# Performance work log

Hardware: AMD Instinct MI355X
Metric: run time of the kernel (lower is better)

## Reference

```python
import jax, jax.numpy as jnp
import numpy as np

B, S, DIM, H = 2, 2048, 1024, 16
DH = DIM // H


def setup_inputs() -> dict:
    key = jax.random.key(0)
    ks = jax.random.split(key, 12)
    sd = 0.02
    inp = {
        "query": jax.random.normal(ks[0], (B, S, DIM), jnp.float32),
        "key": jax.random.normal(ks[1], (B, S, DIM), jnp.float32),
        "value": jax.random.normal(ks[2], (B, S, DIM), jnp.float32),
        "pad_mask": jax.random.randint(ks[3], (B, 1, 1, S), 0, 2, jnp.int32),
        "training_status": 1,
        "Wq": jax.random.normal(ks[4], (DIM, DIM), jnp.float32) * sd,
        "bq": jnp.zeros((DIM,), jnp.float32),
        "Wk": jax.random.normal(ks[5], (DIM, DIM), jnp.float32) * sd,
        "bk": jnp.zeros((DIM,), jnp.float32),
        "Wv": jax.random.normal(ks[6], (DIM, DIM), jnp.float32) * sd,
        "bv": jnp.zeros((DIM,), jnp.float32),
        "Wf": jax.random.normal(ks[7], (DIM, DIM), jnp.float32) * sd,
        "bf": jnp.zeros((DIM,), jnp.float32),
    }
    return inp


def reference(query, key, value, pad_mask, training_status, Wq, bq, Wk, bk, Wv, bv, Wf, bf):
    b, s, _ = query.shape
    # projections, split heads -> [B, H, S, Dh]
    def split_heads(x):
        return x.reshape(b, -1, H, DH).transpose(0, 2, 1, 3)

    q = split_heads(query @ Wq + bq)
    k = split_heads(key @ Wk + bk)
    v = split_heads(value @ Wv + bv)

    # NOTE: original divides by sqrt(Dh) twice (explicit + self.scale) => /Dh
    scores = jnp.einsum("bhqd,bhkd->bhqk", q, k) / jnp.asarray(DH, q.dtype)
    if training_status:
        scores = jnp.where(pad_mask == 0, jnp.asarray(-1e9, scores.dtype), scores)
    attn = jax.nn.softmax(scores, axis=-1)
    out = jnp.einsum("bhqk,bhkd->bhqd", attn, v)  # [B,H,S,Dh]
    out = out.transpose(0, 2, 1, 3).reshape(b, s, DIM)
    return out @ Wf + bf
```

## Files before the change

### kernel.cpp

```cpp
#include <hip/hip_runtime.h>

#define Bn   2
#define Sn   2048
#define DIMn 1024
#define Hn   16
#define DHn  64

typedef unsigned short u16;
typedef unsigned int   u32;

typedef __attribute__((ext_vector_type(8))) __bf16 bf16x8;
typedef __attribute__((ext_vector_type(8))) float  f32x8v;
typedef __attribute__((ext_vector_type(4))) float  f32x4;

__device__ __forceinline__ u16 f2bf(float f) {
    union { float f; u32 u; } v; v.f = f;
    u32 r = v.u + 0x7fffu + ((v.u >> 16) & 1u);
    return (u16)(r >> 16);
}
__device__ __forceinline__ bf16x8 ldfrag(const u16* p) {
    union { uint4 u; bf16x8 v; } x;
    x.u = *(const uint4*)p;
    return x.v;
}
__device__ __forceinline__ uint4 pack8(const u16 h[8]) {
    uint4 r;
    r.x = (u32)h[0] | ((u32)h[1] << 16);
    r.y = (u32)h[2] | ((u32)h[3] << 16);
    r.z = (u32)h[4] | ((u32)h[5] << 16);
    r.w = (u32)h[6] | ((u32)h[7] << 16);
    return r;
}
__device__ __forceinline__ void gl_lds16(const void* g, void* l) {
    __builtin_amdgcn_global_load_lds(
        (const __attribute__((address_space(1))) void*)g,
        (__attribute__((address_space(3))) void*)l, 16, 0, 0);
}
__device__ __forceinline__ void barrier_nodrain() {
    asm volatile("" ::: "memory");
    __builtin_amdgcn_s_barrier();
    asm volatile("" ::: "memory");
}

__global__ __launch_bounds__(256) void prep_weights(
    const float* __restrict__ Wq, const float* __restrict__ Wk,
    const float* __restrict__ Wv, const float* __restrict__ Wf,
    u16* __restrict__ Wt)
{
    __shared__ __align__(16) float tile[64][68];
    const float* W = (blockIdx.z == 0) ? Wq : (blockIdx.z == 1) ? Wk
                   : (blockIdx.z == 2) ? Wv : Wf;
    u16* out = Wt + (size_t)blockIdx.z * DIMn * DIMn;
    const int t = threadIdx.x;
    const int n0 = blockIdx.x * 64, k0 = blockIdx.y * 64;
    const int rr = t >> 4, cc = (t & 15) * 4;
#pragma unroll
    for (int i = 0; i < 4; i++)
        *(float4*)&tile[rr + 16 * i][cc] =
            *(const float4*)(W + (size_t)(k0 + rr + 16 * i) * DIMn + n0 + cc);
    __syncthreads();
#pragma unroll
    for (int e = 0; e < 2; e++) {
        const int ci = 2 * t + e;
        const int n = ci >> 3, kc = ci & 7;
        u16 h[8];
#pragma unroll
        for (int j = 0; j < 8; j++) h[j] = f2bf(tile[kc * 8 + j][n]);
        *(uint4*)(out + (size_t)(n0 + n) * DIMn + k0 + kc * 8) = pack8(h);
    }
}

__global__ __launch_bounds__(256) void gemm_qkv(
    const float* __restrict__ Aq, const float* __restrict__ Ak,
    const float* __restrict__ Av, const u16* __restrict__ Wt,
    const float* __restrict__ bqp, const float* __restrict__ bkp,
    const float* __restrict__ bvp, u16* __restrict__ Qw,
    u16* __restrict__ Kw, u16* __restrict__ VwT)
{
    __shared__ union {
        struct { __align__(16) float Afp[2][64 * 64];
                 __align__(16) u16   Bbf[2][32 * 128]; } s;
        __align__(16) u16 Ep[32][144];
    } L;

    const int f = blockIdx.x;
    const int xcd = f & 7;
    const int q = f >> 3;
    const int z = q >> 5;
    const int rem = q & 31;
    const int yi = rem >> 3, x = rem & 7;
    const int y = xcd * 4 + yi;
    const int m0 = y * 128, n0 = x * 128;

    const float* A    = (z == 0) ? Aq  : (z == 1) ? Ak  : Av;
    const float* bias = (z == 0) ? bqp : (z == 1) ? bkp : bvp;
    const u16* Bt = Wt + (size_t)z * DIMn * DIMn;

    const int t = threadIdx.x;
    const int lane = t & 63, wave = t >> 6;
    const int quad = lane >> 4, l15 = lane & 15;
    const int wm = wave >> 1, wn = wave & 1;

    const float* baseA[4];
#pragma unroll
    for (int s = 0; s < 4; s++) {
        const int c = wave * 16 + s * 4 + quad;
        const int g = c >> 3, qq = (c >> 1) & 3, h = c & 1;
        baseA[s] = A + (size_t)(m0 + g * 16 + l15) * DIMn + qq * 8 + h * 4;
    }
    const u16* baseB[2];
#pragma unroll
    for (int s = 0; s < 2; s++) {
        const int c = wave * 8 + s * 4 + quad;
        const int jg = c >> 2, qq = c & 3;
        baseB[s] = Bt + (size_t)(n0 + jg * 16 + l15) * DIMn + qq * 8;
    }

    auto STAGE = [&](int tt, int buf) {
        const int k0 = tt * 32;
#pragma unroll
        for (int s = 0; s < 4; s++)
            gl_lds16(baseA[s] + k0, &L.s.Afp[buf][(wave * 16 + s * 4) * 64]);
#pragma unroll
        for (int s = 0; s < 2; s++)
            gl_lds16(baseB[s] + k0, &L.s.Bbf[buf][(wave * 8 + s * 4) * 128]);
    };

    f32x4 acc[4][4];
#pragma unroll
    for (int i = 0; i < 4; i++)
#pragma unroll
        for (int j = 0; j < 4; j++) acc[i][j] = (f32x4){0.f, 0.f, 0.f, 0.f};

    const int NT = DIMn / 32;
    STAGE(0, 0);
    STAGE(1, 1);

#pragma unroll 2
    for (int tt = 0; tt < NT; ++tt) {
        const int buf = tt & 1;
        if (tt < NT - 1) asm volatile("s_waitcnt vmcnt(6)" ::: "memory");
        else             asm volatile("s_waitcnt vmcnt(0)" ::: "memory");
        barrier_nodrain();

        bf16x8 a[4], b[4];
#pragma unroll
        for (int i = 0; i < 4; i++) {
            const int g = wm * 4 + i;
            union { struct { f32x4 lo, hi; } p; f32x8v v; } u;
            u.p.lo = *(const f32x4*)&L.s.Afp[buf][(g * 8 + quad * 2 + 0) * 64 + l15 * 4];
            u.p.hi = *(const f32x4*)&L.s.Afp[buf][(g * 8 + quad * 2 + 1) * 64 + l15 * 4];
            a[i] = __builtin_convertvector(u.v, bf16x8);
        }
#pragma unroll
        for (int j = 0; j < 4; j++)
            b[j] = ldfrag(&L.s.Bbf[buf][((wn * 4 + j) * 4 + quad) * 128 + l15 * 8]);
#pragma unroll
        for (int i = 0; i < 4; i++)
#pragma unroll
            for (int j = 0; j < 4; j++)
                acc[i][j] = __builtin_amdgcn_mfma_f32_16x16x32_bf16(a[i], b[j], acc[i][j], 0, 0, 0);

        asm volatile("s_waitcnt lgkmcnt(0)" ::: "memory");
        barrier_nodrain();
        if (tt + 2 < NT) STAGE(tt + 2, buf);
    }

    float bv[4];
#pragma unroll
    for (int j = 0; j < 4; j++) bv[j] = bias[n0 + wn * 64 + j * 16 + l15];

    const int bb = y >> 4;

    if (z < 2) {
        u16* out = (z == 0) ? Qw : Kw;
#pragma unroll
        for (int i = 0; i < 4; i++) {
            __syncthreads();
#pragma unroll
            for (int j = 0; j < 4; j++)
#pragma unroll
                for (int r = 0; r < 4; r++)
                    L.Ep[wm * 16 + quad * 4 + r][wn * 64 + j * 16 + l15] =
                        f2bf(acc[i][j][r] + bv[j]);
            __syncthreads();
#pragma unroll
            for (int e = 0; e < 2; e++) {
                const int ci = t + 256 * e;
                const int row = ci >> 4, c = ci & 15;
                const uint4 v = *(const uint4*)&L.Ep[row][c * 8];
                const int m = m0 + (row >> 4) * 64 + i * 16 + (row & 15);
                const int ss = m & 2047;
                const int n = n0 + c * 8;
                const int hh = n >> 6, dd = n & 63;
                *(uint4*)(out + ((size_t)(bb * Hn + hh) * Sn + ss) * DHn + dd) = v;
            }
        }
    } else {
#pragma unroll
        for (int j = 0; j < 4; j++) {
            __syncthreads();
#pragma unroll
            for (int i = 0; i < 4; i++) {
                u16 h4[4];
#pragma unroll
                for (int r = 0; r < 4; r++) h4[r] = f2bf(acc[i][j][r] + bv[j]);
                uint2 pk;
                pk.x = (u32)h4[0] | ((u32)h4[1] << 16);
                pk.y = (u32)h4[2] | ((u32)h4[3] << 16);
                *(uint2*)&L.Ep[wn * 16 + l15][wm * 64 + i * 16 + quad * 4] = pk;
            }
            __syncthreads();
#pragma unroll
            for (int e = 0; e < 2; e++) {
                const int ci = t + 256 * e;
                const int row = ci >> 4, c = ci & 15;
                const uint4 v = *(const uint4*)&L.Ep[row][c * 8];
                const int n = n0 + (row >> 4) * 64 + j * 16 + (row & 15);
                const int hh = n >> 6, dd = n & 63;
                const int ss = (m0 & 2047) + c * 8;
                *(uint4*)(VwT + ((size_t)(bb * Hn + hh) * DHn + dd) * Sn + ss) = v;
            }
        }
    }
}

__global__ __launch_bounds__(256) void gemm_final(
    const u16* __restrict__ A, const u16* __restrict__ Bt,
    const float* __restrict__ bias, float* __restrict__ out)
{
    __shared__ __align__(16) u16 Abf[3][32 * 128];
    __shared__ __align__(16) u16 Bbf[3][32 * 128];

    const int f = blockIdx.x;
    const int xcd = f & 7, q = f >> 3;
    const int y = xcd * 4 + (q >> 3), x = q & 7;
    const int m0 = y * 128, n0 = x * 128;

    const int t = threadIdx.x;
    const int lane = t & 63, wave = t >> 6;
    const int quad = lane >> 4, l15 = lane & 15;
    const int wm = wave >> 1, wn = wave & 1;

    int arow[2], aq[2];
#pragma unroll
    for (int s = 0; s < 2; s++) {
        const int c = wave * 8 + s * 4 + quad;
        arow[s] = (c >> 2) * 16 + l15;
        aq[s] = c & 3;
    }
    const u16* baseB[2];
#pragma unroll
    for (int s = 0; s < 2; s++) {
        const int c = wave * 8 + s * 4 + quad;
        baseB[s] = Bt + (size_t)(n0 + (c >> 2) * 16 + l15) * DIMn + (c & 3) * 8;
    }

    auto STAGE = [&](int tt, int buf) {
        const int hh = tt >> 1, d64 = (tt & 1) * 32;
#pragma unroll
        for (int s = 0; s < 2; s++) {
            const int m = m0 + arow[s], bb = m >> 11, ss = m & 2047;
            const u16* gp = A + ((size_t)(bb * Hn + hh) * Sn + ss) * DHn + d64 + aq[s] * 8;
            gl_lds16(gp, &Abf[buf][(wave * 8 + s * 4) * 128]);
        }
#pragma unroll
        for (int s = 0; s < 2; s++)
            gl_lds16(baseB[s] + tt * 32, &Bbf[buf][(wave * 8 + s * 4) * 128]);
    };

    f32x4 acc[4][4];
#pragma unroll
    for (int i = 0; i < 4; i++)
#pragma unroll
        for (int j = 0; j < 4; j++) acc[i][j] = (f32x4){0.f, 0.f, 0.f, 0.f};

    const int NT = DIMn / 32;
    STAGE(0, 0);
    STAGE(1, 1);
    STAGE(2, 2);

    int buf = 0;
    for (int tt = 0; tt < NT; ++tt) {
        if (tt < NT - 2)       asm volatile("s_waitcnt vmcnt(8)" ::: "memory");
        else if (tt == NT - 2) asm volatile("s_waitcnt vmcnt(4)" ::: "memory");
        else                   asm volatile("s_waitcnt vmcnt(0)" ::: "memory");
        barrier_nodrain();

        bf16x8 a[4], b[4];
#pragma unroll
        for (int i = 0; i < 4; i++)
            a[i] = ldfrag(&Abf[buf][((wm * 4 + i) * 4 + quad) * 128 + l15 * 8]);
#pragma unroll
        for (int j = 0; j < 4; j++)
            b[j] = ldfrag(&Bbf[buf][((wn * 4 + j) * 4 + quad) * 128 + l15 * 8]);
#pragma unroll
        for (int i = 0; i < 4; i++)
#pragma unroll
            for (int j = 0; j < 4; j++)
                acc[i][j] = __builtin_amdgcn_mfma_f32_16x16x32_bf16(a[i], b[j], acc[i][j], 0, 0, 0);

        asm volatile("s_waitcnt lgkmcnt(0)" ::: "memory");
        barrier_nodrain();
        if (tt + 3 < NT) STAGE(tt + 3, buf);
        buf = (buf == 2) ? 0 : buf + 1;
    }

    float bv[4];
#pragma unroll
    for (int j = 0; j < 4; j++) bv[j] = bias[n0 + wn * 64 + j * 16 + l15];

#pragma unroll
    for (int i = 0; i < 4; i++)
#pragma unroll
        for (int j = 0; j < 4; j++) {
            const int n = n0 + wn * 64 + j * 16 + l15;
#pragma unroll
            for (int r = 0; r < 4; r++) {
                const int m = m0 + wm * 64 + i * 16 + quad * 4 + r;
                out[(size_t)m * DIMn + n] = acc[i][j][r] + bv[j];
            }
        }
}

__global__ __launch_bounds__(256) void attn_mfma(
    const u16* __restrict__ Qw, const u16* __restrict__ Kw,
    const u16* __restrict__ VwT, const int* __restrict__ mask,
    const int* __restrict__ tstat, u16* __restrict__ Aw)
{
    __shared__ __align__(16) u16 Kbf[2][32 * 128];
    __shared__ __align__(16) u16 Vbf[2][32 * 128];
    __shared__ __align__(16) u16 Ps[64 * 64];

    const int f = blockIdx.x;
    const int xcd = f & 7, q = f >> 3;
    const int p = xcd * 4 + (q >> 5);
    const int qt = q & 31;
    const int b = p >> 4, h = p & 15;
    const int q0 = qt * 64;

    const int t = threadIdx.x;
    const int lane = t & 63, wave = t >> 6;
    const int quad = lane >> 4, l15 = lane & 15;
    const bool use_mask = (tstat[0] != 0);
    const size_t slab = (size_t)(b * Hn + h) * Sn * DHn;

    const u16* baseK[2];
    const u16* baseV[2];
#pragma unroll
    for (int s = 0; s < 2; s++) {
        const int c = wave * 8 + s * 4 + quad;
        const int rg = c >> 3, qp = c & 7;
        baseK[s] = Kw  + slab + (size_t)(rg * 16 + l15) * DHn + qp * 8;
        baseV[s] = VwT + slab + (size_t)(rg * 16 + l15) * Sn  + qp * 8;
    }

    {
        const int4* msrc4 = (const int4*)(mask + (size_t)b * Sn);
        int4* mdst4 = (int4*)&Kbf[0][0];
        mdst4[t]       = msrc4[t];
        mdst4[t + 256] = msrc4[t + 256];
    }
    bf16x8 aq[2];
#pragma unroll
    for (int ks = 0; ks < 2; ks++) {
        union { uint4 u; bf16x8 v; } xx;
        xx.u = *(const uint4*)(Qw + slab + (size_t)(q0 + wave * 16 + l15) * DHn + ks * 32 + quad * 8);
        aq[ks] = xx.v;
    }
    __syncthreads();

    u32 mw0 = 0, mw1 = 0, mw2 = 0, mw3 = 0;
    {
        const int* ml = (const int*)&Kbf[0][0];
#pragma unroll
        for (int k = 0; k < 128; k++) {
            const u32 bit = (ml[k * 16 + l15] != 0) ? 1u : 0u;
            if (k < 32)      mw0 |= bit << k;
            else if (k < 64) mw1 |= bit << (k - 32);
            else if (k < 96) mw2 |= bit << (k - 64);
            else             mw3 |= bit << (k - 96);
        }
    }
    __syncthreads();

    auto STAGE = [&](int tt, int buf) {
        const int j0 = tt * 64;
#pragma unroll
        for (int s = 0; s < 2; s++) {
            gl_lds16(baseK[s] + (size_t)j0 * DHn, &Kbf[buf][(wave * 8 + s * 4) * 128]);
            gl_lds16(baseV[s] + j0,               &Vbf[buf][(wave * 8 + s * 4) * 128]);
        }
    };

    float lsum[4] = {0.f, 0.f, 0.f, 0.f};
    f32x4 O[4];
#pragma unroll
    for (int dt = 0; dt < 4; dt++) O[dt] = (f32x4){0.f, 0.f, 0.f, 0.f};

    const int NT = Sn / 64;
    STAGE(0, 0);
    STAGE(1, 1);

#pragma unroll 2
    for (int tt = 0; tt < NT; ++tt) {
        const int buf = tt & 1;
        if (tt < NT - 1) asm volatile("s_waitcnt vmcnt(4)" ::: "memory");
        else             asm volatile("s_waitcnt vmcnt(0)" ::: "memory");
        barrier_nodrain();

        f32x4 s[4];
#pragma unroll
        for (int ct = 0; ct < 4; ct++) s[ct] = (f32x4){0.f, 0.f, 0.f, 0.f};
#pragma unroll
        for (int ct = 0; ct < 4; ct++)
#pragma unroll
            for (int ks = 0; ks < 2; ks++) {
                const bf16x8 bk = ldfrag(&Kbf[buf][(ct * 8 + ks * 4 + quad) * 128 + l15 * 8]);
                s[ct] = __builtin_amdgcn_mfma_f32_16x16x32_bf16(aq[ks], bk, s[ct], 0, 0, 0);
            }

        const int wsel = tt >> 3;
        const u32 cw = (wsel == 0) ? mw0 : (wsel == 1) ? mw1 : (wsel == 2) ? mw2 : mw3;
        const int sh = (tt & 7) * 4;
        u32 mc[4];
#pragma unroll
        for (int ct = 0; ct < 4; ct++)
            mc[ct] = use_mask ? ((cw >> (sh + ct)) & 1u) : 1u;

#pragma unroll
        for (int ct = 0; ct < 4; ct++)
#pragma unroll
            for (int r = 0; r < 4; r++) {
                const float sv = mc[ct] ? s[ct][r] * (1.0f / 64.0f) : -1e9f;
                const float pp = __expf(sv);
                lsum[r] += pp;
                const int prow = wave * 16 + quad * 4 + r;
                Ps[prow * 64 + ((ct * 16 + l15) ^ ((prow & 7) << 3))] = f2bf(pp);
            }
        asm volatile("s_waitcnt lgkmcnt(0)" ::: "memory");

        bf16x8 pa[2];
        const int rrow = wave * 16 + l15;
#pragma unroll
        for (int kc = 0; kc < 2; kc++)
            pa[kc] = ldfrag(&Ps[rrow * 64 + ((kc * 32 + quad * 8) ^ ((l15 & 7) << 3))]);
#pragma unroll
        for (int dt = 0; dt < 4; dt++)
#pragma unroll
            for (int kc = 0; kc < 2; kc++) {
                const bf16x8 bvv = ldfrag(&Vbf[buf][(dt * 8 + kc * 4 + quad) * 128 + l15 * 8]);
                O[dt] = __builtin_amdgcn_mfma_f32_16x16x32_bf16(pa[kc], bvv, O[dt], 0, 0, 0);
            }

        asm volatile("s_waitcnt lgkmcnt(0)" ::: "memory");
        barrier_nodrain();
        if (tt + 2 < NT) STAGE(tt + 2, buf);
    }

#pragma unroll
    for (int r = 0; r < 4; r++) {
#pragma unroll
        for (int off = 1; off < 16; off <<= 1) lsum[r] += __shfl_xor(lsum[r], off);
    }

#pragma unroll
    for (int r = 0; r < 4; r++) {
        const float linv = 1.0f / fmaxf(lsum[r], 1e-30f);
        const int srow = q0 + wave * 16 + quad * 4 + r;
#pragma unroll
        for (int dt = 0; dt < 4; dt++)
            Aw[slab + (size_t)srow * DHn + dt * 16 + l15] = f2bf(O[dt][r] * linv);
    }
}

extern "C" void kernel_launch(void* const* d_in, const int* in_sizes, int n_in,
                              void* d_out, int out_size, void* d_ws, size_t ws_size,
                              hipStream_t stream) {
    const float* query = (const float*)d_in[0];
    const float* key   = (const float*)d_in[1];
    const float* value = (const float*)d_in[2];
    const int*   pmask = (const int*)d_in[3];
    const int*   tstat = (const int*)d_in[4];
    const float* Wq  = (const float*)d_in[5];
    const float* bq  = (const float*)d_in[6];
    const float* Wk  = (const float*)d_in[7];
    const float* bk  = (const float*)d_in[8];
    const float* Wv  = (const float*)d_in[9];
    const float* bv  = (const float*)d_in[10];
    const float* Wf  = (const float*)d_in[11];
    const float* bfb = (const float*)d_in[12];
    float* outp = (float*)d_out;

    const size_t NT = (size_t)Bn * Sn * DIMn;
    u16* Qw  = (u16*)d_ws;
    u16* Kw  = Qw + NT;
    u16* VwT = Kw + NT;
    u16* Wt  = VwT + NT;
    const size_t WSZ = (size_t)DIMn * DIMn;

    prep_weights<<<dim3(16, 16, 4), 256, 0, stream>>>(Wq, Wk, Wv, Wf, Wt);

    gemm_qkv<<<768, 256, 0, stream>>>(query, key, value, Wt, bq, bk, bv, Qw, Kw, VwT);

    attn_mfma<<<1024, 256, 0, stream>>>(Qw, Kw, VwT, pmask, tstat, Qw);

    gemm_final<<<256, 256, 0, stream>>>(Qw, Wt + 3 * WSZ, bfb, outp);
}
```

Baseline: 307.6 us.

## Pre-tile weights, K and V into fragment-contiguous blocks; swizzle A staging; stage attention output

Weights, K and V are now written in a tiled, MFMA-fragment-ordered layout, so each global-to-LDS load in the GEMM and attention kernels reads one contiguous 8KB block per tile instead of strided rows. The fp32 A tile in the QKV GEMM is staged with an XOR swizzle to reduce LDS bank conflicts. The attention epilogue goes through LDS so output rows are written with coalesced 16-byte stores instead of scattered 2-byte stores. The cost is more complex index math in the epilogues, and every producer and consumer must agree on the new layout.

```diff
diff --git a/kernel.cpp b/kernel.cpp
--- a/kernel.cpp
+++ b/kernel.cpp
@@ -50,7 +50,6 @@
     __shared__ __align__(16) float tile[64][68];
     const float* W = (blockIdx.z == 0) ? Wq : (blockIdx.z == 1) ? Wk
                    : (blockIdx.z == 2) ? Wv : Wf;
-    u16* out = Wt + (size_t)blockIdx.z * DIMn * DIMn;
     const int t = threadIdx.x;
     const int n0 = blockIdx.x * 64, k0 = blockIdx.y * 64;
     const int rr = t >> 4, cc = (t & 15) * 4;
@@ -62,11 +61,16 @@
 #pragma unroll
     for (int e = 0; e < 2; e++) {
         const int ci = 2 * t + e;
-        const int n = ci >> 3, kc = ci & 7;
+        const int nn = ci >> 3, kc = ci & 7;
+        const int n = n0 + nn, k = k0 + kc * 8;
         u16 h[8];
 #pragma unroll
-        for (int j = 0; j < 8; j++) h[j] = f2bf(tile[kc * 8 + j][n]);
-        *(uint4*)(out + (size_t)(n0 + n) * DIMn + k0 + kc * 8) = pack8(h);
+        for (int j = 0; j < 8; j++) h[j] = f2bf(tile[kc * 8 + j][nn]);
+        const int X = n >> 7, o = (n >> 4) & 7, l15 = n & 15;
+        const int T = k >> 5, quad = (k >> 3) & 3;
+        const size_t off =
+            ((((size_t)(blockIdx.z * 8 + X) * 32 + T) * 8 + o) * 64 + quad * 16 + l15) * 8;
+        *(uint4*)(Wt + off) = pack8(h);
     }
 }
 
@@ -78,8 +82,8 @@
     u16* __restrict__ Kw, u16* __restrict__ VwT)
 {
     __shared__ union {
-        struct { __align__(16) float Afp[2][64 * 64];
-                 __align__(16) u16   Bbf[2][32 * 128]; } s;
+        struct { __align__(16) float Afp[2][4096];
+                 __align__(16) u16   Bbf[2][4096]; } s;
         __align__(16) u16 Ep[32][144];
     } L;
 
@@ -94,36 +98,29 @@
 
     const float* A    = (z == 0) ? Aq  : (z == 1) ? Ak  : Av;
     const float* bias = (z == 0) ? bqp : (z == 1) ? bkp : bvp;
-    const u16* Bt = Wt + (size_t)z * DIMn * DIMn;
 
     const int t = threadIdx.x;
     const int lane = t & 63, wave = t >> 6;
     const int quad = lane >> 4, l15 = lane & 15;
     const int wm = wave >> 1, wn = wave & 1;
 
+    const int r8 = lane >> 3, c8 = lane & 7;
     const float* baseA[4];
 #pragma unroll
-    for (int s = 0; s < 4; s++) {
-        const int c = wave * 16 + s * 4 + quad;
-        const int g = c >> 3, qq = (c >> 1) & 3, h = c & 1;
-        baseA[s] = A + (size_t)(m0 + g * 16 + l15) * DIMn + qq * 8 + h * 4;
-    }
+    for (int s = 0; s < 4; s++)
+        baseA[s] = A + (size_t)(m0 + (wave * 4 + s) * 8 + r8) * DIMn + ((c8 ^ r8) << 2);
     const u16* baseB[2];
 #pragma unroll
-    for (int s = 0; s < 2; s++) {
-        const int c = wave * 8 + s * 4 + quad;
-        const int jg = c >> 2, qq = c & 3;
-        baseB[s] = Bt + (size_t)(n0 + jg * 16 + l15) * DIMn + qq * 8;
-    }
+    for (int s = 0; s < 2; s++)
+        baseB[s] = Wt + ((size_t)((z * 8 + x) * 32) * 8 + (wave * 2 + s)) * 512 + lane * 8;
 
     auto STAGE = [&](int tt, int buf) {
-        const int k0 = tt * 32;
 #pragma unroll
         for (int s = 0; s < 4; s++)
-            gl_lds16(baseA[s] + k0, &L.s.Afp[buf][(wave * 16 + s * 4) * 64]);
+            gl_lds16(baseA[s] + tt * 32, &L.s.Afp[buf][(wave * 4 + s) * 256]);
 #pragma unroll
         for (int s = 0; s < 2; s++)
-            gl_lds16(baseB[s] + k0, &L.s.Bbf[buf][(wave * 8 + s * 4) * 128]);
+            gl_lds16(baseB[s] + (size_t)tt * 4096, &L.s.Bbf[buf][(wave * 8 + s * 4) * 128]);
     };
 
     f32x4 acc[4][4];
@@ -146,10 +143,11 @@
         bf16x8 a[4], b[4];
 #pragma unroll
         for (int i = 0; i < 4; i++) {
-            const int g = wm * 4 + i;
+            const int lr = wm * 64 + i * 16 + l15;
+            const int rx = lr & 7;
             union { struct { f32x4 lo, hi; } p; f32x8v v; } u;
-            u.p.lo = *(const f32x4*)&L.s.Afp[buf][(g * 8 + quad * 2 + 0) * 64 + l15 * 4];
-            u.p.hi = *(const f32x4*)&L.s.Afp[buf][(g * 8 + quad * 2 + 1) * 64 + l15 * 4];
+            u.p.lo = *(const f32x4*)&L.s.Afp[buf][lr * 32 + (((quad * 2 + 0) ^ rx) << 2)];
+            u.p.hi = *(const f32x4*)&L.s.Afp[buf][lr * 32 + (((quad * 2 + 1) ^ rx) << 2)];
             a[i] = __builtin_convertvector(u.v, bf16x8);
         }
 #pragma unroll
@@ -172,8 +170,7 @@
 
     const int bb = y >> 4;
 
-    if (z < 2) {
-        u16* out = (z == 0) ? Qw : Kw;
+    if (z == 0) {
 #pragma unroll
         for (int i = 0; i < 4; i++) {
             __syncthreads();
@@ -193,7 +190,37 @@
                 const int ss = m & 2047;
                 const int n = n0 + c * 8;
                 const int hh = n >> 6, dd = n & 63;
-                *(uint4*)(out + ((size_t)(bb * Hn + hh) * Sn + ss) * DHn + dd) = v;
+                *(uint4*)(Qw + ((size_t)(bb * Hn + hh) * Sn + ss) * DHn + dd) = v;
+            }
+        }
+    } else if (z == 1) {
+#pragma unroll
+        for (int i = 0; i < 4; i++) {
+            __syncthreads();
+#pragma unroll
+            for (int j = 0; j < 4; j++)
+#pragma unroll
+                for (int r = 0; r < 4; r++)
+                    L.Ep[wm * 16 + quad * 4 + r][wn * 64 + j * 16 + l15] =
+                        f2bf(acc[i][j][r] + bv[j]);
+            __syncthreads();
+#pragma unroll
+            for (int e2 = 0; e2 < 2; e2++) {
+                const int tid = t + 256 * e2;
+                const int l15o = tid & 15;
+                const int qo   = (tid >> 4) & 3;
+                const int k1   = (tid >> 6) & 1;
+                const int c3   = (tid >> 7) & 1;
+                const int w    = (tid >> 8) & 1;
+                const int c    = c3 * 8 + k1 * 4 + qo;
+                const uint4 v = *(const uint4*)&L.Ep[w * 16 + l15o][c * 8];
+                const int ss = (m0 & 2047) + w * 64 + i * 16 + l15o;
+                const int hh = (n0 + c * 8) >> 6;
+                const int jt = ss >> 6;
+                const int o  = i * 2 + k1;
+                const size_t off =
+                    ((((size_t)(bb * Hn + hh) * 32 + jt) * 8 + o) * 64 + qo * 16 + l15o) * 8;
+                *(uint4*)(Kw + off) = v;
             }
         }
     } else {
@@ -212,14 +239,22 @@
             }
             __syncthreads();
 #pragma unroll
-            for (int e = 0; e < 2; e++) {
-                const int ci = t + 256 * e;
-                const int row = ci >> 4, c = ci & 15;
-                const uint4 v = *(const uint4*)&L.Ep[row][c * 8];
-                const int n = n0 + (row >> 4) * 64 + j * 16 + (row & 15);
-                const int hh = n >> 6, dd = n & 63;
-                const int ss = (m0 & 2047) + c * 8;
-                *(uint4*)(VwT + ((size_t)(bb * Hn + hh) * DHn + dd) * Sn + ss) = v;
+            for (int e2 = 0; e2 < 2; e2++) {
+                const int tid = t + 256 * e2;
+                const int l15o = tid & 15;
+                const int qo   = (tid >> 4) & 3;
+                const int k1   = (tid >> 6) & 1;
+                const int c3   = (tid >> 7) & 1;
+                const int w    = (tid >> 8) & 1;
+                const int c    = c3 * 8 + k1 * 4 + qo;
+                const uint4 v = *(const uint4*)&L.Ep[w * 16 + l15o][c * 8];
+                const int n  = n0 + w * 64 + j * 16 + l15o;
+                const int hh = n >> 6;
+                const int jt = ((m0 & 2047) >> 6) + c3;
+                const int o  = j * 2 + k1;
+                const size_t off =
+                    ((((size_t)(bb * Hn + hh) * 32 + jt) * 8 + o) * 64 + qo * 16 + l15o) * 8;
+                *(uint4*)(VwT + off) = v;
             }
         }
     }
@@ -251,10 +286,8 @@
     }
     const u16* baseB[2];
 #pragma unroll
-    for (int s = 0; s < 2; s++) {
-        const int c = wave * 8 + s * 4 + quad;
-        baseB[s] = Bt + (size_t)(n0 + (c >> 2) * 16 + l15) * DIMn + (c & 3) * 8;
-    }
+    for (int s = 0; s < 2; s++)
+        baseB[s] = Bt + ((size_t)(x * 32) * 8 + (wave * 2 + s)) * 512 + lane * 8;
 
     auto STAGE = [&](int tt, int buf) {
         const int hh = tt >> 1, d64 = (tt & 1) * 32;
@@ -266,7 +299,7 @@
         }
 #pragma unroll
         for (int s = 0; s < 2; s++)
-            gl_lds16(baseB[s] + tt * 32, &Bbf[buf][(wave * 8 + s * 4) * 128]);
+            gl_lds16(baseB[s] + (size_t)tt * 4096, &Bbf[buf][(wave * 8 + s * 4) * 128]);
     };
 
     f32x4 acc[4][4];
@@ -345,14 +378,14 @@
     const bool use_mask = (tstat[0] != 0);
     const size_t slab = (size_t)(b * Hn + h) * Sn * DHn;
 
+    const size_t hbase = (size_t)(b * Hn + h) * 32 * 8 * 512;
     const u16* baseK[2];
     const u16* baseV[2];
 #pragma unroll
     for (int s = 0; s < 2; s++) {
-        const int c = wave * 8 + s * 4 + quad;
-        const int rg = c >> 3, qp = c & 7;
-        baseK[s] = Kw  + slab + (size_t)(rg * 16 + l15) * DHn + qp * 8;
-        baseV[s] = VwT + slab + (size_t)(rg * 16 + l15) * Sn  + qp * 8;
+        const int o = wave * 2 + s;
+        baseK[s] = Kw  + hbase + (size_t)o * 512 + lane * 8;
+        baseV[s] = VwT + hbase + (size_t)o * 512 + lane * 8;
     }
 
     {
@@ -385,11 +418,10 @@
     __syncthreads();
 
     auto STAGE = [&](int tt, int buf) {
-        const int j0 = tt * 64;
 #pragma unroll
         for (int s = 0; s < 2; s++) {
-            gl_lds16(baseK[s] + (size_t)j0 * DHn, &Kbf[buf][(wave * 8 + s * 4) * 128]);
-            gl_lds16(baseV[s] + j0,               &Vbf[buf][(wave * 8 + s * 4) * 128]);
+            gl_lds16(baseK[s] + (size_t)tt * 4096, &Kbf[buf][(wave * 8 + s * 4) * 128]);
+            gl_lds16(baseV[s] + (size_t)tt * 4096, &Vbf[buf][(wave * 8 + s * 4) * 128]);
         }
     };
 
@@ -463,14 +495,23 @@
 #pragma unroll
         for (int off = 1; off < 16; off <<= 1) lsum[r] += __shfl_xor(lsum[r], off);
     }
-
-#pragma unroll
-    for (int r = 0; r < 4; r++) {
-        const float linv = 1.0f / fmaxf(lsum[r], 1e-30f);
-        const int srow = q0 + wave * 16 + quad * 4 + r;
+    float linv[4];
+#pragma unroll
+    for (int r = 0; r < 4; r++) linv[r] = 1.0f / fmaxf(lsum[r], 1e-30f);
+
+    __syncthreads();
+#pragma unroll
+    for (int r = 0; r < 4; r++)
 #pragma unroll
         for (int dt = 0; dt < 4; dt++)
-            Aw[slab + (size_t)srow * DHn + dt * 16 + l15] = f2bf(O[dt][r] * linv);
+            Ps[(wave * 16 + quad * 4 + r) * 64 + dt * 16 + l15] = f2bf(O[dt][r] * linv[r]);
+    __syncthreads();
+#pragma unroll
+    for (int e2 = 0; e2 < 2; e2++) {
+        const int tid = t + 256 * e2;
+        const int lr = tid >> 3, c16 = tid & 7;
+        const uint4 v = *(const uint4*)&Ps[lr * 64 + c16 * 8];
+        *(uint4*)(Aw + slab + (size_t)(q0 + lr) * DHn + c16 * 8) = v;
     }
 }
 
```

New measurement: 277.8 us. -9.7%, faster.
